# Optimization experiments

Measured on AMD Instinct MI355X. Metric: run time of the kernel, lower is better.

Reference implementation:

```python
import jax, jax.numpy as jnp
import numpy as np

N = 100000   # num nodes
E = 1200000  # num edges (avg degree ~12)
D = 64       # emb_dim


def setup_inputs() -> dict:
    key = jax.random.key(0)
    k1, k2, k3, k4, k5, k6 = jax.random.split(key, 6)
    x = jax.random.normal(k1, (N, D), dtype=jnp.float32)
    edge_index = jax.random.randint(k2, (2, E), 0, N, dtype=jnp.int64)
    edge_attr = jax.random.normal(k3, (E, D), dtype=jnp.float32)
    W = jax.random.normal(k4, (D, D), dtype=jnp.float32) * 0.05  # Linear weight
    b = jax.random.normal(k5, (D,), dtype=jnp.float32) * 0.05    # Linear bias
    root_emb = jax.random.normal(k6, (D,), dtype=jnp.float32)
    return {"x": x, "edge_index": edge_index, "edge_attr": edge_attr,
            "W": W, "b": b, "root_emb": root_emb}


def reference(x, edge_index, edge_attr, W, b, root_emb):
    n = x.shape[0]
    x = x @ W.T + b  # Linear(emb_dim, emb_dim)
    row, col = edge_index[0], edge_index[1]
    ones_e = jnp.ones(row.shape[0], dtype=x.dtype)
    # degrees initialized to ones then index_add of ones per edge endpoint
    deg_i = 1.0 + jax.ops.segment_sum(ones_e, row, num_segments=n)
    deg_j = 1.0 + jax.ops.segment_sum(ones_e, col, num_segments=n)
    dinv_i = deg_i ** -0.5
    dinv_j = deg_j ** -0.5
    val = dinv_i[row] * dinv_j[col]  # [E] normalized edge weights
    # spmm(adj_t, x) + message_edge both scatter val-weighted terms to `row`;
    # fuse into a single gather->scale->segment_sum pass (identical math).
    agg = jax.ops.segment_sum(val[:, None] * (x[col] + edge_attr), row,
                              num_segments=n)  # [N, D]
    node_feat = jax.nn.relu(agg) + jax.nn.relu(x + root_emb) * (dinv_i * dinv_j)[:, None]
    return node_feat
```

## Files before the change

### kernel.cpp

```cpp
#include <hip/hip_runtime.h>

#define N_NODES 100000
#define N_EDGES 1200000
#define DIM     64
#define SCAN_B  256
#define NB      ((N_NODES + SCAN_B - 1) / SCAN_B)

typedef unsigned short ushort_t;

__device__ inline float bf2f(ushort_t u) {
    return __uint_as_float(((unsigned int)u) << 16);
}
__device__ inline ushort_t f2bf(float f) {
    unsigned int x = __float_as_uint(f);
    unsigned int r = x + 0x7fff + ((x >> 16) & 1);
    return (ushort_t)(r >> 16);
}

__global__ __launch_bounds__(256) void linear_kernel(
        const float* __restrict__ x, const float* __restrict__ W,
        const float* __restrict__ b, ushort_t* __restrict__ xwb) {
    __shared__ float sWt[DIM * (DIM + 1)];
    __shared__ float sx[16][DIM];

    int t = threadIdx.x;
    int row0 = blockIdx.x * 16;

    for (int i = t; i < DIM * DIM; i += 256) {
        int d = i >> 6, k = i & 63;
        sWt[k * (DIM + 1) + d] = W[i];
    }
    {
        int lr = t >> 4, off = (t & 15) << 2;
        const float4 v = *(const float4*)(x + (size_t)(row0 + lr) * DIM + off);
        sx[lr][off + 0] = v.x; sx[lr][off + 1] = v.y;
        sx[lr][off + 2] = v.z; sx[lr][off + 3] = v.w;
    }
    __syncthreads();

    int d  = t & 63;
    int r0 = (t >> 6) * 4;

    float bd = b[d];
    float a0 = bd, a1 = bd, a2 = bd, a3 = bd;
    const float2* x0 = (const float2*)sx[r0 + 0];
    const float2* x1 = (const float2*)sx[r0 + 1];
    const float2* x2 = (const float2*)sx[r0 + 2];
    const float2* x3 = (const float2*)sx[r0 + 3];
    #pragma unroll
    for (int k2 = 0; k2 < DIM / 2; k2++) {
        float w0 = sWt[(2 * k2 + 0) * (DIM + 1) + d];
        float w1 = sWt[(2 * k2 + 1) * (DIM + 1) + d];
        float2 v0 = x0[k2], v1 = x1[k2], v2 = x2[k2], v3 = x3[k2];
        a0 = fmaf(v0.x, w0, a0); a0 = fmaf(v0.y, w1, a0);
        a1 = fmaf(v1.x, w0, a1); a1 = fmaf(v1.y, w1, a1);
        a2 = fmaf(v2.x, w0, a2); a2 = fmaf(v2.y, w1, a2);
        a3 = fmaf(v3.x, w0, a3); a3 = fmaf(v3.y, w1, a3);
    }
    size_t base = (size_t)(row0 + r0) * DIM + d;
    xwb[base + 0 * DIM] = f2bf(a0);
    xwb[base + 1 * DIM] = f2bf(a1);
    xwb[base + 2 * DIM] = f2bf(a2);
    xwb[base + 3 * DIM] = f2bf(a3);
}

__global__ void count_kernel(const int* __restrict__ row, const int* __restrict__ col,
                             int* __restrict__ cnt_r, int* __restrict__ cnt_c) {
    int i = blockIdx.x * blockDim.x + threadIdx.x;
    if (i * 4 >= N_EDGES) return;
    int4 r4 = ((const int4*)row)[i];
    int4 c4 = ((const int4*)col)[i];
    atomicAdd(&cnt_r[r4.x], 1); atomicAdd(&cnt_r[r4.y], 1);
    atomicAdd(&cnt_r[r4.z], 1); atomicAdd(&cnt_r[r4.w], 1);
    atomicAdd(&cnt_c[c4.x], 1); atomicAdd(&cnt_c[c4.y], 1);
    atomicAdd(&cnt_c[c4.z], 1); atomicAdd(&cnt_c[c4.w], 1);
}

__global__ void scan_a(const int* __restrict__ cnt_r, const int* __restrict__ cnt_c,
                       int* __restrict__ offsets, int* __restrict__ partials,
                       float* __restrict__ dinv_i, float* __restrict__ dinv_j) {
    __shared__ int s[SCAN_B];
    int t = threadIdx.x;
    int i = blockIdx.x * SCAN_B + t;
    int v = (i < N_NODES) ? cnt_r[i] : 0;
    if (i < N_NODES) {
        dinv_i[i] = rsqrtf(1.0f + (float)v);
        dinv_j[i] = rsqrtf(1.0f + (float)cnt_c[i]);
    }
    s[t] = v;
    __syncthreads();
    for (int off = 1; off < SCAN_B; off <<= 1) {
        int add = (t >= off) ? s[t - off] : 0;
        __syncthreads();
        s[t] += add;
        __syncthreads();
    }
    if (i < N_NODES) offsets[i] = s[t] - v;
    if (t == SCAN_B - 1) partials[blockIdx.x] = s[t];
}

__global__ void scan_c(int* __restrict__ offsets, const int* __restrict__ partials,
                       int* __restrict__ cursor) {
    __shared__ int sred[SCAN_B];
    int t = threadIdx.x, bid = blockIdx.x;
    int v = 0;
    for (int j = t; j < NB; j += SCAN_B)
        if (j < bid) v += partials[j];
    sred[t] = v;
    __syncthreads();
    for (int off = SCAN_B / 2; off > 0; off >>= 1) {
        if (t < off) sred[t] += sred[t + off];
        __syncthreads();
    }
    int base = sred[0];
    int i = bid * SCAN_B + t;
    if (i < N_NODES) {
        int o = offsets[i] + base;
        offsets[i] = o;
        cursor[i]  = o;
    }
}

__global__ void bin_kernel(const int* __restrict__ row, const int* __restrict__ col,
                           int* __restrict__ cursor, int2* __restrict__ rec) {
    int e = blockIdx.x * blockDim.x + threadIdx.x;
    if (e >= N_EDGES) return;
    int r = row[e], c = col[e];
    int pos = atomicAdd(&cursor[r], 1);
    rec[pos] = make_int2(e, c);
}

__global__ __launch_bounds__(256) void gather_kernel(
        const int* __restrict__ offsets, const int* __restrict__ cnt_r,
        const int2* __restrict__ rec,
        const float* __restrict__ edge_attr, const ushort_t* __restrict__ xwb,
        const float* __restrict__ dinv_i, const float* __restrict__ dinv_j,
        const float* __restrict__ root, float* __restrict__ out) {
    int lane = threadIdx.x & 63;
    int g    = lane >> 4;
    int q    = (lane & 15) << 2;
    int n    = blockIdx.x * 4 + (threadIdx.x >> 6);

    int   start = offsets[n];
    int   cnt   = cnt_r[n];
    float di    = dinv_i[n];

    float4 acc = make_float4(0.f, 0.f, 0.f, 0.f);
    int k = g;
    if (k < cnt) {
        int2    rc = rec[start + k];
        float4  ea = *(const float4*)(edge_attr + (size_t)rc.x * DIM + q);
        ushort4 xu = *(const ushort4*)(xwb + (size_t)rc.y * DIM + q);
        float   vj = dinv_j[rc.y];
        for (;;) {
            int  kn   = k + 4;
            bool more = kn < cnt;
            int2 rcn; float4 ean; ushort4 xun; float vjn;
            if (more) {
                rcn = rec[start + kn];
                ean = *(const float4*)(edge_attr + (size_t)rcn.x * DIM + q);
                xun = *(const ushort4*)(xwb + (size_t)rcn.y * DIM + q);
                vjn = dinv_j[rcn.y];
            }
            float vv = di * vj;
            acc.x = fmaf(vv, ea.x + bf2f(xu.x), acc.x);
            acc.y = fmaf(vv, ea.y + bf2f(xu.y), acc.y);
            acc.z = fmaf(vv, ea.z + bf2f(xu.z), acc.z);
            acc.w = fmaf(vv, ea.w + bf2f(xu.w), acc.w);
            if (!more) break;
            k = kn; ea = ean; xu = xun; vj = vjn;
        }
    }

    acc.x += __shfl_xor(acc.x, 16); acc.y += __shfl_xor(acc.y, 16);
    acc.z += __shfl_xor(acc.z, 16); acc.w += __shfl_xor(acc.w, 16);
    acc.x += __shfl_xor(acc.x, 32); acc.y += __shfl_xor(acc.y, 32);
    acc.z += __shfl_xor(acc.z, 32); acc.w += __shfl_xor(acc.w, 32);

    if (g == 0) {
        float s = di * dinv_j[n];
        const ushort4 xu = *(const ushort4*)(xwb + (size_t)n * DIM + q);
        const float4  rt = *(const float4*)(root + q);
        float4 o;
        o.x = fmaxf(acc.x, 0.f) + fmaxf(bf2f(xu.x) + rt.x, 0.f) * s;
        o.y = fmaxf(acc.y, 0.f) + fmaxf(bf2f(xu.y) + rt.y, 0.f) * s;
        o.z = fmaxf(acc.z, 0.f) + fmaxf(bf2f(xu.z) + rt.z, 0.f) * s;
        o.w = fmaxf(acc.w, 0.f) + fmaxf(bf2f(xu.w) + rt.w, 0.f) * s;
        *(float4*)(out + (size_t)n * DIM + q) = o;
    }
}

extern "C" void kernel_launch(void* const* d_in, const int* in_sizes, int n_in,
                              void* d_out, int out_size, void* d_ws, size_t ws_size,
                              hipStream_t stream) {
    const float* x         = (const float*)d_in[0];
    const int*   edge_idx  = (const int*)d_in[1];
    const float* edge_attr = (const float*)d_in[2];
    const float* W         = (const float*)d_in[3];
    const float* b         = (const float*)d_in[4];
    const float* root_emb  = (const float*)d_in[5];
    float*       out       = (float*)d_out;

    const int* row = edge_idx;
    const int* col = edge_idx + N_EDGES;

    char* ws = (char*)d_ws;
    ushort_t* xwb      = (ushort_t*)ws;   ws += (size_t)N_NODES * DIM * 2;
    int*      cnt_r    = (int*)ws;        ws += (size_t)N_NODES * 4;
    int*      cnt_c    = (int*)ws;        ws += (size_t)N_NODES * 4;
    float*    dinv_i   = (float*)ws;      ws += (size_t)N_NODES * 4;
    float*    dinv_j   = (float*)ws;      ws += (size_t)N_NODES * 4;
    int*      offsets  = (int*)ws;        ws += (size_t)N_NODES * 4;
    int*      cursor   = (int*)ws;        ws += (size_t)N_NODES * 4;
    int*      partials = (int*)ws;        ws += 1024 * 4;
    int2*     rec      = (int2*)ws;       ws += (size_t)N_EDGES * 8;

    hipMemsetAsync(cnt_r, 0, (size_t)N_NODES * 2 * sizeof(int), stream);

    linear_kernel<<<N_NODES / 16, 256, 0, stream>>>(x, W, b, xwb);

    count_kernel<<<(N_EDGES / 4 + 255) / 256, 256, 0, stream>>>(row, col, cnt_r, cnt_c);

    scan_a<<<NB, SCAN_B, 0, stream>>>(cnt_r, cnt_c, offsets, partials, dinv_i, dinv_j);
    scan_c<<<NB, SCAN_B, 0, stream>>>(offsets, partials, cursor);

    bin_kernel<<<(N_EDGES + 255) / 256, 256, 0, stream>>>(row, col, cursor, rec);

    gather_kernel<<<N_NODES / 4, 256, 0, stream>>>(
        offsets, cnt_r, rec, edge_attr, xwb, dinv_i, dinv_j, root_emb, out);
}
```

Measured before the change: 675.6 us.

## Fuse linear and count kernels, record per-edge rank to drop binning atomics

The linear projection and the degree-count pass now run in one launch, split by block index. The count pass also stores the atomic return value as each edge's rank within its row. Binning then computes the slot as offset plus rank with no atomics and handles four edges per thread, so the cursor array goes away. The gather kernel loads the record two steps ahead and hoists the self-term loads to the top; the speculative record read at k+8 can run past the node's range, though it stays inside the workspace.

Result: faster. 599.5 us (-11.3%).

```diff
diff --git a/kernel.cpp b/kernel.cpp
--- a/kernel.cpp
+++ b/kernel.cpp
@@ -5,6 +5,8 @@
 #define DIM     64
 #define SCAN_B  256
 #define NB      ((N_NODES + SCAN_B - 1) / SCAN_B)
+#define LIN_BLOCKS (N_NODES / 16)
+#define CNT_BLOCKS ((N_EDGES / 4 + 255) / 256)
 
 typedef unsigned short ushort_t;
 
@@ -17,15 +19,36 @@
     return (ushort_t)(r >> 16);
 }
 
-__global__ __launch_bounds__(256) void linear_kernel(
+__global__ __launch_bounds__(256) void prep_kernel(
         const float* __restrict__ x, const float* __restrict__ W,
-        const float* __restrict__ b, ushort_t* __restrict__ xwb) {
+        const float* __restrict__ b, ushort_t* __restrict__ xwb,
+        const int* __restrict__ row, const int* __restrict__ col,
+        int* __restrict__ cnt_r, int* __restrict__ cnt_c,
+        int* __restrict__ rank) {
     __shared__ float sWt[DIM * (DIM + 1)];
     __shared__ float sx[16][DIM];
 
     int t = threadIdx.x;
+
+    if (blockIdx.x >= LIN_BLOCKS) {
+        int i = (blockIdx.x - LIN_BLOCKS) * 256 + t;
+        if (i * 4 >= N_EDGES) return;
+        int4 r4 = ((const int4*)row)[i];
+        int4 c4 = ((const int4*)col)[i];
+        int4 rk;
+        rk.x = atomicAdd(&cnt_r[r4.x], 1);
+        rk.y = atomicAdd(&cnt_r[r4.y], 1);
+        rk.z = atomicAdd(&cnt_r[r4.z], 1);
+        rk.w = atomicAdd(&cnt_r[r4.w], 1);
+        ((int4*)rank)[i] = rk;
+        atomicAdd(&cnt_c[c4.x], 1);
+        atomicAdd(&cnt_c[c4.y], 1);
+        atomicAdd(&cnt_c[c4.z], 1);
+        atomicAdd(&cnt_c[c4.w], 1);
+        return;
+    }
+
     int row0 = blockIdx.x * 16;
-
     for (int i = t; i < DIM * DIM; i += 256) {
         int d = i >> 6, k = i & 63;
         sWt[k * (DIM + 1) + d] = W[i];
@@ -64,18 +87,6 @@
     xwb[base + 3 * DIM] = f2bf(a3);
 }
 
-__global__ void count_kernel(const int* __restrict__ row, const int* __restrict__ col,
-                             int* __restrict__ cnt_r, int* __restrict__ cnt_c) {
-    int i = blockIdx.x * blockDim.x + threadIdx.x;
-    if (i * 4 >= N_EDGES) return;
-    int4 r4 = ((const int4*)row)[i];
-    int4 c4 = ((const int4*)col)[i];
-    atomicAdd(&cnt_r[r4.x], 1); atomicAdd(&cnt_r[r4.y], 1);
-    atomicAdd(&cnt_r[r4.z], 1); atomicAdd(&cnt_r[r4.w], 1);
-    atomicAdd(&cnt_c[c4.x], 1); atomicAdd(&cnt_c[c4.y], 1);
-    atomicAdd(&cnt_c[c4.z], 1); atomicAdd(&cnt_c[c4.w], 1);
-}
-
 __global__ void scan_a(const int* __restrict__ cnt_r, const int* __restrict__ cnt_c,
                        int* __restrict__ offsets, int* __restrict__ partials,
                        float* __restrict__ dinv_i, float* __restrict__ dinv_j) {
@@ -99,8 +110,7 @@
     if (t == SCAN_B - 1) partials[blockIdx.x] = s[t];
 }
 
-__global__ void scan_c(int* __restrict__ offsets, const int* __restrict__ partials,
-                       int* __restrict__ cursor) {
+__global__ void scan_c(int* __restrict__ offsets, const int* __restrict__ partials) {
     __shared__ int sred[SCAN_B];
     int t = threadIdx.x, bid = blockIdx.x;
     int v = 0;
@@ -114,20 +124,22 @@
     }
     int base = sred[0];
     int i = bid * SCAN_B + t;
-    if (i < N_NODES) {
-        int o = offsets[i] + base;
-        offsets[i] = o;
-        cursor[i]  = o;
-    }
+    if (i < N_NODES) offsets[i] += base;
 }
 
 __global__ void bin_kernel(const int* __restrict__ row, const int* __restrict__ col,
-                           int* __restrict__ cursor, int2* __restrict__ rec) {
-    int e = blockIdx.x * blockDim.x + threadIdx.x;
-    if (e >= N_EDGES) return;
-    int r = row[e], c = col[e];
-    int pos = atomicAdd(&cursor[r], 1);
-    rec[pos] = make_int2(e, c);
+                           const int* __restrict__ rank, const int* __restrict__ offsets,
+                           int2* __restrict__ rec) {
+    int i = blockIdx.x * blockDim.x + threadIdx.x;
+    if (i * 4 >= N_EDGES) return;
+    int4 r4 = ((const int4*)row)[i];
+    int4 c4 = ((const int4*)col)[i];
+    int4 k4 = ((const int4*)rank)[i];
+    int e = i * 4;
+    rec[offsets[r4.x] + k4.x] = make_int2(e + 0, c4.x);
+    rec[offsets[r4.y] + k4.y] = make_int2(e + 1, c4.y);
+    rec[offsets[r4.z] + k4.z] = make_int2(e + 2, c4.z);
+    rec[offsets[r4.w] + k4.w] = make_int2(e + 3, c4.w);
 }
 
 __global__ __launch_bounds__(256) void gather_kernel(
@@ -145,22 +157,27 @@
     int   cnt   = cnt_r[n];
     float di    = dinv_i[n];
 
+    const ushort4 xun0 = *(const ushort4*)(xwb + (size_t)n * DIM + q);
+    const float4  rt   = *(const float4*)(root + q);
+    const float   vj0  = dinv_j[n];
+
     float4 acc = make_float4(0.f, 0.f, 0.f, 0.f);
     int k = g;
     if (k < cnt) {
-        int2    rc = rec[start + k];
-        float4  ea = *(const float4*)(edge_attr + (size_t)rc.x * DIM + q);
-        ushort4 xu = *(const ushort4*)(xwb + (size_t)rc.y * DIM + q);
-        float   vj = dinv_j[rc.y];
+        int2 rcB = rec[start + k];
+        int2 rcC = rec[start + k + 4];
+        float4  ea = *(const float4*)(edge_attr + (size_t)rcB.x * DIM + q);
+        ushort4 xu = *(const ushort4*)(xwb + (size_t)rcB.y * DIM + q);
+        float   vj = dinv_j[rcB.y];
         for (;;) {
             int  kn   = k + 4;
             bool more = kn < cnt;
-            int2 rcn; float4 ean; ushort4 xun; float vjn;
+            int2 rcD  = rec[start + k + 8];
+            float4 ean; ushort4 xun; float vjn;
             if (more) {
-                rcn = rec[start + kn];
-                ean = *(const float4*)(edge_attr + (size_t)rcn.x * DIM + q);
-                xun = *(const ushort4*)(xwb + (size_t)rcn.y * DIM + q);
-                vjn = dinv_j[rcn.y];
+                ean = *(const float4*)(edge_attr + (size_t)rcC.x * DIM + q);
+                xun = *(const ushort4*)(xwb + (size_t)rcC.y * DIM + q);
+                vjn = dinv_j[rcC.y];
             }
             float vv = di * vj;
             acc.x = fmaf(vv, ea.x + bf2f(xu.x), acc.x);
@@ -168,7 +185,7 @@
             acc.z = fmaf(vv, ea.z + bf2f(xu.z), acc.z);
             acc.w = fmaf(vv, ea.w + bf2f(xu.w), acc.w);
             if (!more) break;
-            k = kn; ea = ean; xu = xun; vj = vjn;
+            k = kn; ea = ean; xu = xun; vj = vjn; rcC = rcD;
         }
     }
 
@@ -178,14 +195,12 @@
     acc.z += __shfl_xor(acc.z, 32); acc.w += __shfl_xor(acc.w, 32);
 
     if (g == 0) {
-        float s = di * dinv_j[n];
-        const ushort4 xu = *(const ushort4*)(xwb + (size_t)n * DIM + q);
-        const float4  rt = *(const float4*)(root + q);
+        float s = di * vj0;
         float4 o;
-        o.x = fmaxf(acc.x, 0.f) + fmaxf(bf2f(xu.x) + rt.x, 0.f) * s;
-        o.y = fmaxf(acc.y, 0.f) + fmaxf(bf2f(xu.y) + rt.y, 0.f) * s;
-        o.z = fmaxf(acc.z, 0.f) + fmaxf(bf2f(xu.z) + rt.z, 0.f) * s;
-        o.w = fmaxf(acc.w, 0.f) + fmaxf(bf2f(xu.w) + rt.w, 0.f) * s;
+        o.x = fmaxf(acc.x, 0.f) + fmaxf(bf2f(xun0.x) + rt.x, 0.f) * s;
+        o.y = fmaxf(acc.y, 0.f) + fmaxf(bf2f(xun0.y) + rt.y, 0.f) * s;
+        o.z = fmaxf(acc.z, 0.f) + fmaxf(bf2f(xun0.z) + rt.z, 0.f) * s;
+        o.w = fmaxf(acc.w, 0.f) + fmaxf(bf2f(xun0.w) + rt.w, 0.f) * s;
         *(float4*)(out + (size_t)n * DIM + q) = o;
     }
 }
@@ -211,20 +226,19 @@
     float*    dinv_i   = (float*)ws;      ws += (size_t)N_NODES * 4;
     float*    dinv_j   = (float*)ws;      ws += (size_t)N_NODES * 4;
     int*      offsets  = (int*)ws;        ws += (size_t)N_NODES * 4;
-    int*      cursor   = (int*)ws;        ws += (size_t)N_NODES * 4;
     int*      partials = (int*)ws;        ws += 1024 * 4;
+    int*      rank     = (int*)ws;        ws += (size_t)N_EDGES * 4;
     int2*     rec      = (int2*)ws;       ws += (size_t)N_EDGES * 8;
 
     hipMemsetAsync(cnt_r, 0, (size_t)N_NODES * 2 * sizeof(int), stream);
 
-    linear_kernel<<<N_NODES / 16, 256, 0, stream>>>(x, W, b, xwb);
-
-    count_kernel<<<(N_EDGES / 4 + 255) / 256, 256, 0, stream>>>(row, col, cnt_r, cnt_c);
+    prep_kernel<<<LIN_BLOCKS + CNT_BLOCKS, 256, 0, stream>>>(
+        x, W, b, xwb, row, col, cnt_r, cnt_c, rank);
 
     scan_a<<<NB, SCAN_B, 0, stream>>>(cnt_r, cnt_c, offsets, partials, dinv_i, dinv_j);
-    scan_c<<<NB, SCAN_B, 0, stream>>>(offsets, partials, cursor);
-
-    bin_kernel<<<(N_EDGES + 255) / 256, 256, 0, stream>>>(row, col, cursor, rec);
+    scan_c<<<NB, SCAN_B, 0, stream>>>(offsets, partials);
+
+    bin_kernel<<<CNT_BLOCKS, 256, 0, stream>>>(row, col, rank, offsets, rec);
 
     gather_kernel<<<N_NODES / 4, 256, 0, stream>>>(
         offsets, cnt_r, rec, edge_attr, xwb, dinv_i, dinv_j, root_emb, out);
```
